# Optimization experiments

Measured on AMD Instinct MI355X. Metric: run time of the kernel, lower is better.

The kernel has to match this reference:

```python
import jax, jax.numpy as jnp
import numpy as np

C = 256

def setup_inputs() -> dict:
    key = jax.random.key(0)
    k1, k2, k3, k4, k5 = jax.random.split(key, 5)
    x = jax.random.normal(k1, (4, C, 64, 64), dtype=jnp.float32)
    # conv1x1 weights stored as (out, in) matrices
    w_qkv = jax.random.normal(k2, (3 * C, C), dtype=jnp.float32) * (1.0 / np.sqrt(C))
    b_qkv = jax.random.normal(k3, (3 * C,), dtype=jnp.float32) * 0.01
    w_out = jax.random.normal(k4, (C, C), dtype=jnp.float32) * (1.0 / np.sqrt(C))
    b_out = jax.random.normal(k5, (C,), dtype=jnp.float32) * 0.01
    return {"x": x, "w_qkv": w_qkv, "b_qkv": b_qkv, "w_out": w_out, "b_out": b_out}

def reference(x, w_qkv, b_qkv, w_out, b_out):
    b, c, h, w = x.shape
    # norm = Identity. conv1x1 == channel matmul
    qkv = jnp.einsum('bchw,oc->bohw', x, w_qkv) + b_qkv[None, :, None, None]
    q, k, v = jnp.split(qkv, 3, axis=1)  # each (b, c, h, w)
    q = q.reshape(b, c, h * w).transpose(0, 2, 1)  # (b, hw, c)
    k = k.reshape(b, c, h * w)                      # (b, c, hw)
    v = v.reshape(b, c, h * w).transpose(0, 2, 1)  # (b, hw, c)
    scores = jnp.einsum('bnc,bcm->bnm', q, k) * (c ** -0.5)  # (b, hw, hw)
    attn = jax.nn.softmax(scores, axis=-1)
    out = jnp.einsum('bnm,bmc->bnc', attn, v)  # (b, hw, c)
    out = out.transpose(0, 2, 1).reshape(b, c, h, w)
    out = jnp.einsum('bchw,oc->bohw', out, w_out) + b_out[None, :, None, None]
    return out + x
```

## Files before the change

### kernel.cpp

```cpp
#include <hip/hip_runtime.h>
#include <hip/hip_bf16.h>
#include <hip/hip_fp16.h>
#include <math.h>

typedef short s16x8 __attribute__((ext_vector_type(8)));
typedef float f32x4 __attribute__((ext_vector_type(4)));
typedef float f32x16 __attribute__((ext_vector_type(16)));
typedef unsigned short u16x4 __attribute__((ext_vector_type(4)));
typedef unsigned int u32x4 __attribute__((ext_vector_type(4)));

#define CCH 256
#define SEQ 4096
#define NB 4
#define KVB 64

static __device__ __forceinline__ unsigned short f2bf(float f) {
  union { float f; unsigned int u; } v; v.f = f;
  unsigned int u = v.u;
  unsigned int r = u + 0x7FFFu + ((u >> 16) & 1u);
  return (unsigned short)(r >> 16);
}

static __device__ __forceinline__ void gl16(const void* g, void* l) {
  __builtin_amdgcn_global_load_lds(
      (const __attribute__((address_space(1))) void*)g,
      (__attribute__((address_space(3))) void*)l, 16, 0, 0);
}

static __device__ __forceinline__ unsigned int cvt_pk_bf16(float lo, float hi) {
  unsigned int w;
  asm("v_cvt_pk_bf16_f32 %0, %1, %2" : "=v"(w) : "v"(lo), "v"(hi));
  return w;
}

__global__ __launch_bounds__(256) void cvt_wall(
    const float* __restrict__ wqkv, const float* __restrict__ wout,
    unsigned short* __restrict__ wqkb, unsigned short* __restrict__ wob)
{
  int bid = blockIdx.x;
  const float* src;
  unsigned short* dst;
  int i;
  if (bid < 192) { src = wqkv; dst = wqkb; i = bid * 256 + threadIdx.x; }
  else           { src = wout; dst = wob;  i = (bid - 192) * 256 + threadIdx.x; }
  float4 v = ((const float4*)src)[i];
  u16x4 r;
  r.x = f2bf(v.x); r.y = f2bf(v.y); r.z = f2bf(v.z); r.w = f2bf(v.w);
  ((u16x4*)dst)[i] = r;
}

__global__ __launch_bounds__(256) void cvt_x(const float* __restrict__ x,
                                             unsigned short* __restrict__ xb) {
  __shared__ unsigned short T[64][72];
  int b = blockIdx.z, ct = blockIdx.y, st = blockIdx.x;
  int c0 = ct * 64, s0 = st * 64;
  int tid = threadIdx.x;
  #pragma unroll
  for (int i = 0; i < 4; i++) {
    int idx = tid + i * 256;
    int cr = idx >> 4, c4 = idx & 15;
    float4 v = *(const float4*)&x[((size_t)b * CCH + c0 + cr) * SEQ + s0 + c4 * 4];
    #pragma unroll
    for (int j = 0; j < 4; j++) {
      int s = c4 * 4 + j;
      int colp = cr ^ ((((s) >> 1) & 7) << 3);
      float fv = (j == 0) ? v.x : (j == 1) ? v.y : (j == 2) ? v.z : v.w;
      T[s][colp] = f2bf(fv);
    }
  }
  __syncthreads();
  #pragma unroll
  for (int i = 0; i < 2; i++) {
    int idx = tid + i * 256;
    int sr = idx >> 3, ch = idx & 7;
    int chp = ch ^ ((sr >> 1) & 7);
    s16x8 v = *(const s16x8*)&T[sr][chp * 8];
    *(s16x8*)&xb[((size_t)b * SEQ + s0 + sr) * CCH + c0 + ch * 8] = v;
  }
}

__global__ __launch_bounds__(256) void qk_proj(
    const unsigned short* __restrict__ xb, const unsigned short* __restrict__ wqkb,
    const float* __restrict__ bias,
    unsigned short* __restrict__ qb, unsigned short* __restrict__ kb)
{
  int b = blockIdx.y, st = blockIdx.x;
  int tid = threadIdx.x, w = tid >> 6, l = tid & 63, l15 = l & 15, lg = l >> 4;
  int row0 = st * 32 + (w & 1) * 16;
  int osel = w >> 1;

  const unsigned short* xp = xb + ((size_t)b * SEQ + row0 + l15) * CCH + lg * 8;
  s16x8 af[8];
  #pragma unroll
  for (int t = 0; t < 8; t++) af[t] = *(const s16x8*)(xp + t * 32);

  unsigned short* dst = osel ? kb : qb;
  #pragma unroll
  for (int ot = 0; ot < 16; ot++) {
    int orow = osel * 256 + ot * 16;
    f32x4 acc = (f32x4){0.f, 0.f, 0.f, 0.f};
    #pragma unroll
    for (int t = 0; t < 8; t++) {
      s16x8 wf = *(const s16x8*)&wqkb[(size_t)(orow + l15) * CCH + t * 32 + lg * 8];
      acc = __builtin_amdgcn_mfma_f32_16x16x32_bf16(af[t], wf, acc, 0, 0, 0);
    }
    float bi = bias[orow + l15];
    int ch = ot * 16 + l15;
    #pragma unroll
    for (int r = 0; r < 4; r++) {
      int srow = row0 + lg * 4 + r;
      dst[((size_t)b * SEQ + srow) * CCH + ch] = f2bf(acc[r] + bi);
    }
  }
}

__global__ __launch_bounds__(256) void v_proj(
    const unsigned short* __restrict__ xb, const unsigned short* __restrict__ wqkb,
    const float* __restrict__ bias, unsigned short* __restrict__ vb)
{
  int b = blockIdx.y, st = blockIdx.x;
  int tid = threadIdx.x, w = tid >> 6, l = tid & 63, l15 = l & 15, lg = l >> 4;
  int sbase = st * 32, obase = w * 64;

  f32x4 acc[4][2];
  #pragma unroll
  for (int i = 0; i < 4; i++)
    #pragma unroll
    for (int j = 0; j < 2; j++) acc[i][j] = (f32x4){0.f, 0.f, 0.f, 0.f};

  const unsigned short* xrow = xb + ((size_t)b * SEQ + sbase) * CCH;
  #pragma unroll
  for (int kt = 0; kt < 8; kt++) {
    s16x8 afr[4], bfr[2];
    #pragma unroll
    for (int ot = 0; ot < 4; ot++)
      afr[ot] = *(const s16x8*)&wqkb[(size_t)(512 + obase + ot * 16 + l15) * CCH + kt * 32 + lg * 8];
    #pragma unroll
    for (int sj = 0; sj < 2; sj++)
      bfr[sj] = *(const s16x8*)&xrow[(size_t)(sj * 16 + l15) * CCH + kt * 32 + lg * 8];
    #pragma unroll
    for (int ot = 0; ot < 4; ot++)
      #pragma unroll
      for (int sj = 0; sj < 2; sj++)
        acc[ot][sj] = __builtin_amdgcn_mfma_f32_16x16x32_bf16(afr[ot], bfr[sj], acc[ot][sj], 0, 0, 0);
  }

  #pragma unroll
  for (int ot = 0; ot < 4; ot++) {
    #pragma unroll
    for (int r = 0; r < 4; r++) {
      int o = obase + ot * 16 + lg * 4 + r;
      float bi = bias[512 + o];
      #pragma unroll
      for (int sj = 0; sj < 2; sj++) {
        int s = sbase + sj * 16 + l15;
        vb[((size_t)b * CCH + o) * SEQ + s] = f2bf(acc[ot][sj][r] + bi);
      }
    }
  }
}

template<int NSPLIT_>
__global__ __launch_bounds__(512, 2) void attn_kernel(
    const unsigned short* __restrict__ qb,
    const unsigned short* __restrict__ kb,
    const unsigned short* __restrict__ vb,
    __half* __restrict__ pacc, float* __restrict__ llp)
{
  constexpr int KVLEN_ = SEQ / NSPLIT_;
  constexpr int NT_ = KVLEN_ / KVB;
  __shared__ __align__(16) unsigned short Ks[2][KVB * CCH];
  __shared__ __align__(16) unsigned short Vs[2][CCH * KVB];

  int b = blockIdx.z, kvh = blockIdx.y, qt = blockIdx.x;
  int tid = threadIdx.x, w = tid >> 6, l = tid & 63;
  int l31 = l & 31, lh = l >> 5;
  int s7 = l31 & 7;

  int qrow0 = qt * 256 + w * 32;
  const unsigned short* qptr = qb + ((size_t)b * SEQ + qrow0 + l31) * CCH + lh * 8;
  s16x8 qf[16];
  #pragma unroll
  for (int t = 0; t < 16; t++) qf[t] = *(const s16x8*)(qptr + t * 16);

  f32x16 oacc[8];
  #pragma unroll
  for (int i = 0; i < 8; i++)
    #pragma unroll
    for (int j = 0; j < 16; j++) oacc[i][j] = 0.f;
  float ll = 0.f;

  int koff0 = (tid >> 5) * CCH + (((tid & 31) ^ ((tid >> 5) & 7)) * 8);
  int voff0 = (tid >> 3) * SEQ + (((tid & 7) ^ ((tid >> 3) & 7)) * 8);
  const unsigned short* kbb = kb + (size_t)b * SEQ * CCH + (size_t)kvh * KVLEN_ * CCH;
  const unsigned short* vbb = vb + (size_t)b * CCH * SEQ + kvh * KVLEN_;

  auto stage = [&](int bf_, int kv) {
    #pragma unroll
    for (int i = 0; i < 4; i++)
      gl16(kbb + (size_t)kv * KVB * CCH + koff0 + i * 16 * CCH, &Ks[bf_][(i * 512 + tid) * 8]);
    #pragma unroll
    for (int i = 0; i < 4; i++)
      gl16(vbb + kv * KVB + voff0 + (size_t)i * 64 * SEQ, &Vs[bf_][(i * 512 + tid) * 8]);
  };

  stage(0, 0);
  __syncthreads();

  int buf = 0;
  for (int kv = 0; kv < NT_; kv++) {
    if (kv + 1 < NT_) stage(buf ^ 1, kv + 1);

    #pragma unroll
    for (int h = 0; h < 2; h++) {
      f32x16 sacc;
      #pragma unroll
      for (int i = 0; i < 16; i++) sacc[i] = 0.f;
      __builtin_amdgcn_s_setprio(1);
      #pragma unroll
      for (int st = 0; st < 16; st++) {
        s16x8 kf = *(const s16x8*)&Ks[buf][(h * 32 + l31) * CCH + (((st * 2 + lh) ^ s7) * 8)];
        sacc = __builtin_amdgcn_mfma_f32_32x32x16_bf16(kf, qf[st], sacc, 0, 0, 0);
      }
      __builtin_amdgcn_s_setprio(0);

      unsigned int pw[8];
      #pragma unroll
      for (int r = 0; r < 8; r++) {
        float p0 = __builtin_amdgcn_exp2f(fmaf(sacc[2 * r],     0.09016844f, -11.5415602f));
        float p1 = __builtin_amdgcn_exp2f(fmaf(sacc[2 * r + 1], 0.09016844f, -11.5415602f));
        ll += p0 + p1;
        pw[r] = cvt_pk_bf16(p0, p1);
      }
      asm volatile("v_permlane32_swap_b32 %0, %1" : "+v"(pw[0]), "+v"(pw[2]));
      asm volatile("v_permlane32_swap_b32 %0, %1" : "+v"(pw[1]), "+v"(pw[3]));
      asm volatile("v_permlane32_swap_b32 %0, %1" : "+v"(pw[4]), "+v"(pw[6]));
      asm volatile("v_permlane32_swap_b32 %0, %1" : "+v"(pw[5]), "+v"(pw[7]));
      u32x4 pa0u = {pw[0], pw[1], pw[2], pw[3]};
      u32x4 pa1u = {pw[4], pw[5], pw[6], pw[7]};
      s16x8 pa0 = *(s16x8*)&pa0u;
      s16x8 pa1 = *(s16x8*)&pa1u;

      __builtin_amdgcn_s_setprio(1);
      #pragma unroll
      for (int dt = 0; dt < 8; dt++) {
        int base = (dt * 32 + l31) * KVB;
        s16x8 vf0 = *(const s16x8*)&Vs[buf][base + (((h * 4 + lh) ^ s7) * 8)];
        oacc[dt] = __builtin_amdgcn_mfma_f32_32x32x16_bf16(pa0, vf0, oacc[dt], 0, 0, 0);
        s16x8 vf1 = *(const s16x8*)&Vs[buf][base + (((h * 4 + 2 + lh) ^ s7) * 8)];
        oacc[dt] = __builtin_amdgcn_mfma_f32_32x32x16_bf16(pa1, vf1, oacc[dt], 0, 0, 0);
      }
      __builtin_amdgcn_s_setprio(0);
    }

    __syncthreads();
    buf ^= 1;
  }

  ll += __shfl_xor(ll, 32);
  size_t pbase = (size_t)(b * NSPLIT_ + kvh) * SEQ;
  if (lh == 0) llp[pbase + qrow0 + l31] = ll;
  __half* pb_ = pacc + (pbase + qrow0) * CCH + l31;
  #pragma unroll
  for (int rg = 0; rg < 4; rg++)
    #pragma unroll
    for (int j = 0; j < 4; j++) {
      int qr = j + 8 * rg + 4 * lh;
      #pragma unroll
      for (int dt = 0; dt < 8; dt++)
        pb_[(size_t)qr * CCH + dt * 32] = __float2half(oacc[dt][rg * 4 + j]);
    }
}

template<int NSPLIT_>
__global__ __launch_bounds__(256) void combine(
    const __half* __restrict__ pacc, const float* __restrict__ llp,
    unsigned short* __restrict__ aob)
{
  int idx = blockIdx.x * 256 + threadIdx.x;
  int c4 = idx & 63;
  int srow = idx >> 6;
  int b = srow >> 12, s = srow & 4095;
  float den = 0.f;
  float acc[4] = {0.f, 0.f, 0.f, 0.f};
  #pragma unroll
  for (int k = 0; k < NSPLIT_; k++) {
    size_t pb = (size_t)(b * NSPLIT_ + k) * SEQ + s;
    den += llp[pb];
    const __half* p = pacc + pb * CCH + c4 * 4;
    #pragma unroll
    for (int j = 0; j < 4; j++) acc[j] += __half2float(p[j]);
  }
  float inv = 1.f / den;
  u16x4 r;
  #pragma unroll
  for (int j = 0; j < 4; j++) ((unsigned short*)&r)[j] = f2bf(acc[j] * inv);
  *(u16x4*)&aob[((size_t)b * SEQ + s) * CCH + c4 * 4] = r;
}

__global__ __launch_bounds__(256) void out_proj(
    const unsigned short* __restrict__ aob, const unsigned short* __restrict__ wb,
    const float* __restrict__ bias, const float* __restrict__ x,
    float* __restrict__ out)
{
  int b = blockIdx.y, st = blockIdx.x;
  int tid = threadIdx.x, w = tid >> 6, l = tid & 63, l15 = l & 15, lg = l >> 4;
  int sbase = st * 32, obase = w * 64;

  f32x4 acc[4][2];
  #pragma unroll
  for (int i = 0; i < 4; i++)
    #pragma unroll
    for (int j = 0; j < 2; j++) acc[i][j] = (f32x4){0.f, 0.f, 0.f, 0.f};

  const unsigned short* aorow = aob + ((size_t)b * SEQ + sbase) * CCH;
  #pragma unroll
  for (int kt = 0; kt < 8; kt++) {
    s16x8 af[4], bfr[2];
    #pragma unroll
    for (int ot = 0; ot < 4; ot++)
      af[ot] = *(const s16x8*)&wb[(obase + ot * 16 + l15) * CCH + kt * 32 + lg * 8];
    #pragma unroll
    for (int sj = 0; sj < 2; sj++)
      bfr[sj] = *(const s16x8*)&aorow[(size_t)(sj * 16 + l15) * CCH + kt * 32 + lg * 8];
    #pragma unroll
    for (int ot = 0; ot < 4; ot++)
      #pragma unroll
      for (int sj = 0; sj < 2; sj++)
        acc[ot][sj] = __builtin_amdgcn_mfma_f32_16x16x32_bf16(af[ot], bfr[sj], acc[ot][sj], 0, 0, 0);
  }

  #pragma unroll
  for (int ot = 0; ot < 4; ot++) {
    #pragma unroll
    for (int r = 0; r < 4; r++) {
      int o = obase + ot * 16 + lg * 4 + r;
      float bi = bias[o];
      #pragma unroll
      for (int sj = 0; sj < 2; sj++) {
        int s = sbase + sj * 16 + l15;
        size_t idx = ((size_t)b * CCH + o) * SEQ + s;
        out[idx] = acc[ot][sj][r] + bi + x[idx];
      }
    }
  }
}

extern "C" void kernel_launch(void* const* d_in, const int* in_sizes, int n_in,
                              void* d_out, int out_size, void* d_ws, size_t ws_size,
                              hipStream_t stream) {
  const float* x     = (const float*)d_in[0];
  const float* w_qkv = (const float*)d_in[1];
  const float* b_qkv = (const float*)d_in[2];
  const float* w_out = (const float*)d_in[3];
  const float* b_out = (const float*)d_in[4];
  float* out = (float*)d_out;

  char* ws = (char*)d_ws;
  unsigned short* xbp  = (unsigned short*)(ws);
  unsigned short* qbp  = (unsigned short*)(ws + ((size_t)8 << 20));
  unsigned short* kbp  = (unsigned short*)(ws + ((size_t)16 << 20));
  unsigned short* vbp  = (unsigned short*)(ws + ((size_t)24 << 20));
  unsigned short* aob  = (unsigned short*)(ws + ((size_t)32 << 20));
  unsigned short* wqkb = (unsigned short*)(ws + ((size_t)40 << 20));
  unsigned short* wob  = (unsigned short*)(ws + ((size_t)40 << 20) + (512u << 10));
  float*          llp  = (float*)(ws + ((size_t)41 << 20));
  __half*         pacc = (__half*)(ws + ((size_t)42 << 20));

  cvt_wall<<<dim3(256), 256, 0, stream>>>(w_qkv, w_out, wqkb, wob);
  cvt_x<<<dim3(64, 4, NB), 256, 0, stream>>>(x, xbp);
  qk_proj<<<dim3(128, NB), 256, 0, stream>>>(xbp, wqkb, b_qkv, qbp, kbp);
  v_proj<<<dim3(128, NB), 256, 0, stream>>>(xbp, wqkb, b_qkv, vbp);

  bool split4 = ws_size >= ((size_t)76 << 20);
  if (split4) {
    attn_kernel<4><<<dim3(16, 4, NB), 512, 0, stream>>>(qbp, kbp, vbp, pacc, llp);
    combine<4><<<dim3(4096), 256, 0, stream>>>(pacc, llp, aob);
  } else {
    attn_kernel<2><<<dim3(16, 2, NB), 512, 0, stream>>>(qbp, kbp, vbp, pacc, llp);
    combine<2><<<dim3(4096), 256, 0, stream>>>(pacc, llp, aob);
  }
  out_proj<<<dim3(128, NB), 256, 0, stream>>>(aob, wob, b_out, x, out);
}
```

Measured before the change: 163.0 us.

## Fuse prep and projection kernels, fold split combine into out_proj, reswizzle LDS

Merges the weight and x bf16 conversions into one prep launch and the Q/K and V projections into one 512-thread kernel. The split-KV combine is folded into out_proj, which now reads the fp16 partials directly and normalizes them, so the intermediate attention-output buffer disappears. The attention kernel's K/V LDS XOR swizzle now also mixes in higher row bits to reduce bank conflicts. Fusing removes launches and a global round trip. In exchange, out_proj redundantly reloads and reduces partials once per wave, four times per block.

```diff
diff --git a/kernel.cpp b/kernel.cpp
--- a/kernel.cpp
+++ b/kernel.cpp
@@ -33,28 +33,28 @@
   return w;
 }
 
-__global__ __launch_bounds__(256) void cvt_wall(
-    const float* __restrict__ wqkv, const float* __restrict__ wout,
-    unsigned short* __restrict__ wqkb, unsigned short* __restrict__ wob)
+__global__ __launch_bounds__(256) void prep(
+    const float* __restrict__ x, const float* __restrict__ wqkv,
+    const float* __restrict__ wout,
+    unsigned short* __restrict__ xb, unsigned short* __restrict__ wqkb,
+    unsigned short* __restrict__ wob)
 {
+  __shared__ unsigned short T[64][72];
   int bid = blockIdx.x;
-  const float* src;
-  unsigned short* dst;
-  int i;
-  if (bid < 192) { src = wqkv; dst = wqkb; i = bid * 256 + threadIdx.x; }
-  else           { src = wout; dst = wob;  i = (bid - 192) * 256 + threadIdx.x; }
-  float4 v = ((const float4*)src)[i];
-  u16x4 r;
-  r.x = f2bf(v.x); r.y = f2bf(v.y); r.z = f2bf(v.z); r.w = f2bf(v.w);
-  ((u16x4*)dst)[i] = r;
-}
-
-__global__ __launch_bounds__(256) void cvt_x(const float* __restrict__ x,
-                                             unsigned short* __restrict__ xb) {
-  __shared__ unsigned short T[64][72];
-  int b = blockIdx.z, ct = blockIdx.y, st = blockIdx.x;
+  int tid = threadIdx.x;
+  if (bid < 256) {
+    const float* src; unsigned short* dst; int i;
+    if (bid < 192) { src = wqkv; dst = wqkb; i = bid * 256 + tid; }
+    else           { src = wout; dst = wob;  i = (bid - 192) * 256 + tid; }
+    float4 v = ((const float4*)src)[i];
+    u16x4 r;
+    r.x = f2bf(v.x); r.y = f2bf(v.y); r.z = f2bf(v.z); r.w = f2bf(v.w);
+    ((u16x4*)dst)[i] = r;
+    return;
+  }
+  int v_ = bid - 256;
+  int st = v_ & 63, ct = (v_ >> 6) & 3, b = v_ >> 8;
   int c0 = ct * 64, s0 = st * 64;
-  int tid = threadIdx.x;
   #pragma unroll
   for (int i = 0; i < 4; i++) {
     int idx = tid + i * 256;
@@ -74,87 +74,82 @@
     int idx = tid + i * 256;
     int sr = idx >> 3, ch = idx & 7;
     int chp = ch ^ ((sr >> 1) & 7);
-    s16x8 v = *(const s16x8*)&T[sr][chp * 8];
-    *(s16x8*)&xb[((size_t)b * SEQ + s0 + sr) * CCH + c0 + ch * 8] = v;
-  }
-}
-
-__global__ __launch_bounds__(256) void qk_proj(
+    s16x8 vv = *(const s16x8*)&T[sr][chp * 8];
+    *(s16x8*)&xb[((size_t)b * SEQ + s0 + sr) * CCH + c0 + ch * 8] = vv;
+  }
+}
+
+__global__ __launch_bounds__(512) void qkv_proj(
     const unsigned short* __restrict__ xb, const unsigned short* __restrict__ wqkb,
     const float* __restrict__ bias,
-    unsigned short* __restrict__ qb, unsigned short* __restrict__ kb)
+    unsigned short* __restrict__ qb, unsigned short* __restrict__ kb,
+    unsigned short* __restrict__ vb)
 {
   int b = blockIdx.y, st = blockIdx.x;
   int tid = threadIdx.x, w = tid >> 6, l = tid & 63, l15 = l & 15, lg = l >> 4;
-  int row0 = st * 32 + (w & 1) * 16;
-  int osel = w >> 1;
-
-  const unsigned short* xp = xb + ((size_t)b * SEQ + row0 + l15) * CCH + lg * 8;
-  s16x8 af[8];
-  #pragma unroll
-  for (int t = 0; t < 8; t++) af[t] = *(const s16x8*)(xp + t * 32);
-
-  unsigned short* dst = osel ? kb : qb;
-  #pragma unroll
-  for (int ot = 0; ot < 16; ot++) {
-    int orow = osel * 256 + ot * 16;
-    f32x4 acc = (f32x4){0.f, 0.f, 0.f, 0.f};
-    #pragma unroll
-    for (int t = 0; t < 8; t++) {
-      s16x8 wf = *(const s16x8*)&wqkb[(size_t)(orow + l15) * CCH + t * 32 + lg * 8];
-      acc = __builtin_amdgcn_mfma_f32_16x16x32_bf16(af[t], wf, acc, 0, 0, 0);
-    }
-    float bi = bias[orow + l15];
-    int ch = ot * 16 + l15;
-    #pragma unroll
-    for (int r = 0; r < 4; r++) {
-      int srow = row0 + lg * 4 + r;
-      dst[((size_t)b * SEQ + srow) * CCH + ch] = f2bf(acc[r] + bi);
-    }
-  }
-}
-
-__global__ __launch_bounds__(256) void v_proj(
-    const unsigned short* __restrict__ xb, const unsigned short* __restrict__ wqkb,
-    const float* __restrict__ bias, unsigned short* __restrict__ vb)
-{
-  int b = blockIdx.y, st = blockIdx.x;
-  int tid = threadIdx.x, w = tid >> 6, l = tid & 63, l15 = l & 15, lg = l >> 4;
-  int sbase = st * 32, obase = w * 64;
-
-  f32x4 acc[4][2];
-  #pragma unroll
-  for (int i = 0; i < 4; i++)
-    #pragma unroll
-    for (int j = 0; j < 2; j++) acc[i][j] = (f32x4){0.f, 0.f, 0.f, 0.f};
-
-  const unsigned short* xrow = xb + ((size_t)b * SEQ + sbase) * CCH;
-  #pragma unroll
-  for (int kt = 0; kt < 8; kt++) {
-    s16x8 afr[4], bfr[2];
-    #pragma unroll
-    for (int ot = 0; ot < 4; ot++)
-      afr[ot] = *(const s16x8*)&wqkb[(size_t)(512 + obase + ot * 16 + l15) * CCH + kt * 32 + lg * 8];
-    #pragma unroll
-    for (int sj = 0; sj < 2; sj++)
-      bfr[sj] = *(const s16x8*)&xrow[(size_t)(sj * 16 + l15) * CCH + kt * 32 + lg * 8];
-    #pragma unroll
-    for (int ot = 0; ot < 4; ot++)
+
+  if (w < 4) {
+    int row0 = st * 32 + (w & 1) * 16;
+    int osel = w >> 1;
+    const unsigned short* xp = xb + ((size_t)b * SEQ + row0 + l15) * CCH + lg * 8;
+    s16x8 af[8];
+    #pragma unroll
+    for (int t = 0; t < 8; t++) af[t] = *(const s16x8*)(xp + t * 32);
+
+    unsigned short* dst = osel ? kb : qb;
+    #pragma unroll
+    for (int ot = 0; ot < 16; ot++) {
+      int orow = osel * 256 + ot * 16;
+      f32x4 acc = (f32x4){0.f, 0.f, 0.f, 0.f};
+      #pragma unroll
+      for (int t = 0; t < 8; t++) {
+        s16x8 wf = *(const s16x8*)&wqkb[(size_t)(orow + l15) * CCH + t * 32 + lg * 8];
+        acc = __builtin_amdgcn_mfma_f32_16x16x32_bf16(af[t], wf, acc, 0, 0, 0);
+      }
+      float bi = bias[orow + l15];
+      int ch = ot * 16 + l15;
+      #pragma unroll
+      for (int r = 0; r < 4; r++) {
+        int srow = row0 + lg * 4 + r;
+        dst[((size_t)b * SEQ + srow) * CCH + ch] = f2bf(acc[r] + bi);
+      }
+    }
+  } else {
+    int sbase = st * 32, obase = (w - 4) * 64;
+    f32x4 acc[4][2];
+    #pragma unroll
+    for (int i = 0; i < 4; i++)
+      #pragma unroll
+      for (int j = 0; j < 2; j++) acc[i][j] = (f32x4){0.f, 0.f, 0.f, 0.f};
+
+    const unsigned short* xrow = xb + ((size_t)b * SEQ + sbase) * CCH;
+    #pragma unroll
+    for (int kt = 0; kt < 8; kt++) {
+      s16x8 afr[4], bfr[2];
+      #pragma unroll
+      for (int ot = 0; ot < 4; ot++)
+        afr[ot] = *(const s16x8*)&wqkb[(size_t)(512 + obase + ot * 16 + l15) * CCH + kt * 32 + lg * 8];
       #pragma unroll
       for (int sj = 0; sj < 2; sj++)
-        acc[ot][sj] = __builtin_amdgcn_mfma_f32_16x16x32_bf16(afr[ot], bfr[sj], acc[ot][sj], 0, 0, 0);
-  }
-
-  #pragma unroll
-  for (int ot = 0; ot < 4; ot++) {
-    #pragma unroll
-    for (int r = 0; r < 4; r++) {
-      int o = obase + ot * 16 + lg * 4 + r;
-      float bi = bias[512 + o];
-      #pragma unroll
-      for (int sj = 0; sj < 2; sj++) {
-        int s = sbase + sj * 16 + l15;
-        vb[((size_t)b * CCH + o) * SEQ + s] = f2bf(acc[ot][sj][r] + bi);
+        bfr[sj] = *(const s16x8*)&xrow[(size_t)(sj * 16 + l15) * CCH + kt * 32 + lg * 8];
+      #pragma unroll
+      for (int ot = 0; ot < 4; ot++)
+        #pragma unroll
+        for (int sj = 0; sj < 2; sj++)
+          acc[ot][sj] = __builtin_amdgcn_mfma_f32_16x16x32_bf16(afr[ot], bfr[sj], acc[ot][sj], 0, 0, 0);
+    }
+
+    #pragma unroll
+    for (int ot = 0; ot < 4; ot++) {
+      #pragma unroll
+      for (int r = 0; r < 4; r++) {
+        int o = obase + ot * 16 + lg * 4 + r;
+        float bi = bias[512 + o];
+        #pragma unroll
+        for (int sj = 0; sj < 2; sj++) {
+          int s = sbase + sj * 16 + l15;
+          vb[((size_t)b * CCH + o) * SEQ + s] = f2bf(acc[ot][sj][r] + bi);
+        }
       }
     }
   }
@@ -175,7 +170,7 @@
   int b = blockIdx.z, kvh = blockIdx.y, qt = blockIdx.x;
   int tid = threadIdx.x, w = tid >> 6, l = tid & 63;
   int l31 = l & 31, lh = l >> 5;
-  int s7 = l31 & 7;
+  int s7 = l31 & 7, lq = l31 >> 3;
 
   int qrow0 = qt * 256 + w * 32;
   const unsigned short* qptr = qb + ((size_t)b * SEQ + qrow0 + l31) * CCH + lh * 8;
@@ -190,18 +185,24 @@
     for (int j = 0; j < 16; j++) oacc[i][j] = 0.f;
   float ll = 0.f;
 
-  int koff0 = (tid >> 5) * CCH + (((tid & 31) ^ ((tid >> 5) & 7)) * 8);
-  int voff0 = (tid >> 3) * SEQ + (((tid & 7) ^ ((tid >> 3) & 7)) * 8);
   const unsigned short* kbb = kb + (size_t)b * SEQ * CCH + (size_t)kvh * KVLEN_ * CCH;
   const unsigned short* vbb = vb + (size_t)b * CCH * SEQ + kvh * KVLEN_;
 
   auto stage = [&](int bf_, int kv) {
     #pragma unroll
-    for (int i = 0; i < 4; i++)
-      gl16(kbb + (size_t)kv * KVB * CCH + koff0 + i * 16 * CCH, &Ks[bf_][(i * 512 + tid) * 8]);
-    #pragma unroll
-    for (int i = 0; i < 4; i++)
-      gl16(vbb + kv * KVB + voff0 + (size_t)i * 64 * SEQ, &Vs[bf_][(i * 512 + tid) * 8]);
+    for (int i = 0; i < 4; i++) {
+      int row = (tid >> 5) + i * 16;
+      int gk = (row ^ (row >> 3)) & 7;
+      gl16(kbb + (size_t)kv * KVB * CCH + (size_t)row * CCH + (((tid & 31) ^ gk) * 8),
+           &Ks[bf_][(i * 512 + tid) * 8]);
+    }
+    #pragma unroll
+    for (int i = 0; i < 4; i++) {
+      int ch = (tid >> 3) + i * 64;
+      int gv = (ch ^ (ch >> 3)) & 7;
+      gl16(vbb + kv * KVB + (size_t)ch * SEQ + (((tid & 7) ^ gv) * 8),
+           &Vs[bf_][(i * 512 + tid) * 8]);
+    }
   };
 
   stage(0, 0);
@@ -213,13 +214,14 @@
 
     #pragma unroll
     for (int h = 0; h < 2; h++) {
+      int gk = s7 ^ ((h * 4 + lq) & 7);
       f32x16 sacc;
       #pragma unroll
       for (int i = 0; i < 16; i++) sacc[i] = 0.f;
       __builtin_amdgcn_s_setprio(1);
       #pragma unroll
       for (int st = 0; st < 16; st++) {
-        s16x8 kf = *(const s16x8*)&Ks[buf][(h * 32 + l31) * CCH + (((st * 2 + lh) ^ s7) * 8)];
+        s16x8 kf = *(const s16x8*)&Ks[buf][(h * 32 + l31) * CCH + (((st * 2 + lh) ^ gk) * 8)];
         sacc = __builtin_amdgcn_mfma_f32_32x32x16_bf16(kf, qf[st], sacc, 0, 0, 0);
       }
       __builtin_amdgcn_s_setprio(0);
@@ -244,10 +246,11 @@
       __builtin_amdgcn_s_setprio(1);
       #pragma unroll
       for (int dt = 0; dt < 8; dt++) {
+        int gv = s7 ^ ((dt * 4 + lq) & 7);
         int base = (dt * 32 + l31) * KVB;
-        s16x8 vf0 = *(const s16x8*)&Vs[buf][base + (((h * 4 + lh) ^ s7) * 8)];
+        s16x8 vf0 = *(const s16x8*)&Vs[buf][base + (((h * 4 + lh) ^ gv) * 8)];
         oacc[dt] = __builtin_amdgcn_mfma_f32_32x32x16_bf16(pa0, vf0, oacc[dt], 0, 0, 0);
-        s16x8 vf1 = *(const s16x8*)&Vs[buf][base + (((h * 4 + 2 + lh) ^ s7) * 8)];
+        s16x8 vf1 = *(const s16x8*)&Vs[buf][base + (((h * 4 + 2 + lh) ^ gv) * 8)];
         oacc[dt] = __builtin_amdgcn_mfma_f32_32x32x16_bf16(pa1, vf1, oacc[dt], 0, 0, 0);
       }
       __builtin_amdgcn_s_setprio(0);
@@ -272,34 +275,10 @@
     }
 }
 
-template<int NSPLIT_>
-__global__ __launch_bounds__(256) void combine(
+template<int NS>
+__global__ __launch_bounds__(256) void out_proj(
     const __half* __restrict__ pacc, const float* __restrict__ llp,
-    unsigned short* __restrict__ aob)
-{
-  int idx = blockIdx.x * 256 + threadIdx.x;
-  int c4 = idx & 63;
-  int srow = idx >> 6;
-  int b = srow >> 12, s = srow & 4095;
-  float den = 0.f;
-  float acc[4] = {0.f, 0.f, 0.f, 0.f};
-  #pragma unroll
-  for (int k = 0; k < NSPLIT_; k++) {
-    size_t pb = (size_t)(b * NSPLIT_ + k) * SEQ + s;
-    den += llp[pb];
-    const __half* p = pacc + pb * CCH + c4 * 4;
-    #pragma unroll
-    for (int j = 0; j < 4; j++) acc[j] += __half2float(p[j]);
-  }
-  float inv = 1.f / den;
-  u16x4 r;
-  #pragma unroll
-  for (int j = 0; j < 4; j++) ((unsigned short*)&r)[j] = f2bf(acc[j] * inv);
-  *(u16x4*)&aob[((size_t)b * SEQ + s) * CCH + c4 * 4] = r;
-}
-
-__global__ __launch_bounds__(256) void out_proj(
-    const unsigned short* __restrict__ aob, const unsigned short* __restrict__ wb,
+    const unsigned short* __restrict__ wb,
     const float* __restrict__ bias, const float* __restrict__ x,
     float* __restrict__ out)
 {
@@ -307,13 +286,22 @@
   int tid = threadIdx.x, w = tid >> 6, l = tid & 63, l15 = l & 15, lg = l >> 4;
   int sbase = st * 32, obase = w * 64;
 
+  float inv[2];
+  #pragma unroll
+  for (int sj = 0; sj < 2; sj++) {
+    int s = sbase + sj * 16 + l15;
+    float den = 0.f;
+    #pragma unroll
+    for (int k = 0; k < NS; k++) den += llp[(size_t)(b * NS + k) * SEQ + s];
+    inv[sj] = 1.f / den;
+  }
+
   f32x4 acc[4][2];
   #pragma unroll
   for (int i = 0; i < 4; i++)
     #pragma unroll
     for (int j = 0; j < 2; j++) acc[i][j] = (f32x4){0.f, 0.f, 0.f, 0.f};
 
-  const unsigned short* aorow = aob + ((size_t)b * SEQ + sbase) * CCH;
   #pragma unroll
   for (int kt = 0; kt < 8; kt++) {
     s16x8 af[4], bfr[2];
@@ -321,8 +309,34 @@
     for (int ot = 0; ot < 4; ot++)
       af[ot] = *(const s16x8*)&wb[(obase + ot * 16 + l15) * CCH + kt * 32 + lg * 8];
     #pragma unroll
-    for (int sj = 0; sj < 2; sj++)
-      bfr[sj] = *(const s16x8*)&aorow[(size_t)(sj * 16 + l15) * CCH + kt * 32 + lg * 8];
+    for (int sj = 0; sj < 2; sj++) {
+      int s = sbase + sj * 16 + l15;
+      float facc[8] = {0.f, 0.f, 0.f, 0.f, 0.f, 0.f, 0.f, 0.f};
+      #pragma unroll
+      for (int k = 0; k < NS; k++) {
+        const __half* p = pacc + ((size_t)(b * NS + k) * SEQ + s) * CCH + kt * 32 + lg * 8;
+        u16x4 h0 = *(const u16x4*)(p);
+        u16x4 h1 = *(const u16x4*)(p + 4);
+        #pragma unroll
+        for (int j = 0; j < 4; j++) {
+          facc[j]     += __half2float(*(const __half*)&((const unsigned short*)&h0)[j]);
+          facc[4 + j] += __half2float(*(const __half*)&((const unsigned short*)&h1)[j]);
+        }
+      }
+      u16x4 lo, hi;
+      #pragma unroll
+      for (int j = 0; j < 4; j++) {
+        ((unsigned short*)&lo)[j] = f2bf(facc[j] * inv[sj]);
+        ((unsigned short*)&hi)[j] = f2bf(facc[4 + j] * inv[sj]);
+      }
+      u32x4 packed = {*(unsigned int*)&((unsigned short*)&lo)[0] | ((unsigned int)((unsigned short*)&lo)[1] << 16),
+                      0, 0, 0};
+      unsigned short tmp[8];
+      #pragma unroll
+      for (int j = 0; j < 4; j++) { tmp[j] = ((unsigned short*)&lo)[j]; tmp[4 + j] = ((unsigned short*)&hi)[j]; }
+      bfr[sj] = *(s16x8*)tmp;
+      (void)packed;
+    }
     #pragma unroll
     for (int ot = 0; ot < 4; ot++)
       #pragma unroll
@@ -361,24 +375,20 @@
   unsigned short* qbp  = (unsigned short*)(ws + ((size_t)8 << 20));
   unsigned short* kbp  = (unsigned short*)(ws + ((size_t)16 << 20));
   unsigned short* vbp  = (unsigned short*)(ws + ((size_t)24 << 20));
-  unsigned short* aob  = (unsigned short*)(ws + ((size_t)32 << 20));
   unsigned short* wqkb = (unsigned short*)(ws + ((size_t)40 << 20));
   unsigned short* wob  = (unsigned short*)(ws + ((size_t)40 << 20) + (512u << 10));
   float*          llp  = (float*)(ws + ((size_t)41 << 20));
   __half*         pacc = (__half*)(ws + ((size_t)42 << 20));
 
-  cvt_wall<<<dim3(256), 256, 0, stream>>>(w_qkv, w_out, wqkb, wob);
-  cvt_x<<<dim3(64, 4, NB), 256, 0, stream>>>(x, xbp);
-  qk_proj<<<dim3(128, NB), 256, 0, stream>>>(xbp, wqkb, b_qkv, qbp, kbp);
-  v_proj<<<dim3(128, NB), 256, 0, stream>>>(xbp, wqkb, b_qkv, vbp);
+  prep<<<dim3(1280), 256, 0, stream>>>(x, w_qkv, w_out, xbp, wqkb, wob);
+  qkv_proj<<<dim3(128, NB), 512, 0, stream>>>(xbp, wqkb, b_qkv, qbp, kbp, vbp);
 
   bool split4 = ws_size >= ((size_t)76 << 20);
   if (split4) {
     attn_kernel<4><<<dim3(16, 4, NB), 512, 0, stream>>>(qbp, kbp, vbp, pacc, llp);
-    combine<4><<<dim3(4096), 256, 0, stream>>>(pacc, llp, aob);
+    out_proj<4><<<dim3(128, NB), 256, 0, stream>>>(pacc, llp, wob, b_out, x, out);
   } else {
     attn_kernel<2><<<dim3(16, 2, NB), 512, 0, stream>>>(qbp, kbp, vbp, pacc, llp);
-    combine<2><<<dim3(4096), 256, 0, stream>>>(pacc, llp, aob);
-  }
-  out_proj<<<dim3(128, NB), 256, 0, stream>>>(aob, wob, b_out, x, out);
-}
+    out_proj<2><<<dim3(128, NB), 256, 0, stream>>>(pacc, llp, wob, b_out, x, out);
+  }
+}
```

After: 174.9 us. 1.07x slower.
